# Kernel tuning notes

Hardware: AMD Instinct MI355X
Metric: run time of the kernel (lower is better)

## Reference

```python
import jax, jax.numpy as jnp
import numpy as np
from jax import lax

GRID_SIZE = 5
SPLINE_ORDER = 3
GRID_RANGE = (-1.0, 1.0)
# (cin, cout, kernel, stride, pad) per KAN conv layer
CONVS = [(3, 16, 7, 2, 3), (16, 32, 3, 2, 1), (32, 64, 3, 2, 1)]


def make_grid(in_features):
    # uniform extended knot grid: (in_features, grid_size + 2*order + 1)
    h = (GRID_RANGE[1] - GRID_RANGE[0]) / GRID_SIZE
    g = jnp.arange(-SPLINE_ORDER, GRID_SIZE + SPLINE_ORDER + 1, dtype=jnp.float32) * h + GRID_RANGE[0]
    return jnp.broadcast_to(g, (in_features, g.shape[0]))


def b_splines(x, grid):
    # x: (N, in)  ->  (N, in, grid_size + order) via Cox-de Boor recursion
    x = x[..., None]
    bases = ((x >= grid[:, :-1]) & (x < grid[:, 1:])).astype(x.dtype)
    for k in range(1, SPLINE_ORDER + 1):
        left = (x - grid[:, : -(k + 1)]) / (grid[:, k:-1] - grid[:, : -(k + 1)])
        right = (grid[:, k + 1:] - x) / (grid[:, k + 1:] - grid[:, 1:-k])
        bases = left * bases[..., :-1] + right * bases[..., 1:]
    return bases


def kan_linear(x, grid, base_w, spline_w, spline_scaler):
    # base path: silu(x) @ W_base^T ; spline path: B(x) contracted with scaled spline coeffs
    base = jax.nn.silu(x) @ base_w.T
    bsp = b_splines(x, grid)                      # (N, in, K)
    scaled = spline_w * spline_scaler[..., None]  # (out, in, K)
    spline = jnp.einsum('nik,oik->no', bsp, scaled)
    return base + spline


def max_pool_2x2(x):
    return lax.reduce_window(x, -jnp.inf, lax.max, (1, 1, 2, 2), (1, 1, 2, 2), 'VALID')


def setup_inputs() -> dict:
    key = jax.random.key(0)
    ks = jax.random.split(key, 16)
    inp = {'x': jax.random.uniform(ks[0], (8, 3, 224, 224), dtype=jnp.float32)}
    dims = [(16, 147), (32, 144), (64, 288)]
    i = 1
    for li, (out_f, in_f) in enumerate(dims):
        inp[f'bw{li}'] = jax.random.normal(ks[i], (out_f, in_f), jnp.float32) / np.sqrt(in_f); i += 1
        inp[f'sw{li}'] = jax.random.normal(ks[i], (out_f, in_f, GRID_SIZE + SPLINE_ORDER), jnp.float32) * 0.1; i += 1
        inp[f'sc{li}'] = 1.0 + 0.1 * jax.random.normal(ks[i], (out_f, in_f), jnp.float32); i += 1
    inp['bwc'] = jax.random.normal(ks[i], (200, 64), jnp.float32) / 8.0; i += 1
    inp['swc'] = jax.random.normal(ks[i], (200, 64, GRID_SIZE + SPLINE_ORDER), jnp.float32) * 0.1; i += 1
    inp['scc'] = 1.0 + 0.1 * jax.random.normal(ks[i], (200, 64), jnp.float32)
    return inp


def reference(x, bw0, sw0, sc0, bw1, sw1, sc1, bw2, sw2, sc2, bwc, swc, scc):
    params = [(bw0, sw0, sc0), (bw1, sw1, sc1), (bw2, sw2, sc2)]
    h = x
    for i, (cin, cout, k, s, p) in enumerate(CONVS):
        # unfold: (B, cin*k*k, Ho, Wo) with channel-major patch ordering (matches torch unfold)
        patches = lax.conv_general_dilated_patches(
            h, (k, k), (s, s), [(p, p), (p, p)],
            dimension_numbers=('NCHW', 'OIHW', 'NCHW'))
        B, F_, Ho, Wo = patches.shape
        flat = patches.transpose(0, 2, 3, 1).reshape(-1, F_)  # (B*Ho*Wo, cin*k*k)
        y = kan_linear(flat, make_grid(F_), *params[i])
        h = y.reshape(B, Ho, Wo, cout).transpose(0, 3, 1, 2)
        h = jax.nn.relu(h)
        if i < len(CONVS) - 1:
            h = max_pool_2x2(h)
    h = h.mean(axis=(2, 3))  # adaptive avg pool to 1x1 + flatten -> (B, 64)
    return kan_linear(h, make_grid(h.shape[1]), bwc, swc, scc)
```

## Files before the change

kernel.cpp:

```cpp
#include <hip/hip_runtime.h>

#define DEV __device__ __forceinline__

typedef _Float16 f16x8 __attribute__((ext_vector_type(8)));
typedef float f32x4 __attribute__((ext_vector_type(4)));
typedef unsigned int u32x4 __attribute__((ext_vector_type(4)));

DEV f16x8 kan_feats8(float x) {
    const float sil = x / (1.0f + __expf(-x));
    const float k0 = (float)(-3) * 0.4f - 1.0f;
    const float t = (x - k0) * 2.5f;
    const float mf = floorf(t);
    const int m = (int)mf;
    const float u = t - mf, v = 1.0f - u;
    const float u2 = u * u, u3 = u2 * u;
    const float N0 = v * v * v * (1.0f / 6.0f);
    const float N1 = (3.0f * u3 - 6.0f * u2 + 4.0f) * (1.0f / 6.0f);
    const float N2 = (-3.0f * u3 + 3.0f * u2 + 3.0f * u + 1.0f) * (1.0f / 6.0f);
    const float N3 = u3 * (1.0f / 6.0f);
    f16x8 g;
    g[0] = (_Float16)sil;
#pragma unroll
    for (int jj = 0; jj < 6; ++jj) {
        const int j = jj + 2;
        float val = 0.0f;
        val = (m == j + 3) ? N0 : val;
        val = (m == j + 2) ? N1 : val;
        val = (m == j + 1) ? N2 : val;
        val = (m == j)     ? N3 : val;
        g[1 + jj] = (_Float16)val;
    }
    g[7] = (_Float16)0.0f;
    return g;
}

DEV void kan_feats9(float x, float* f) {
    f[0] = x / (1.0f + __expf(-x));
    const float k0 = (float)(-3) * 0.4f - 1.0f;
    const float t = (x - k0) * 2.5f;
    const float mf = floorf(t);
    const int m = (int)mf;
    const float u = t - mf, v = 1.0f - u;
    const float u2 = u * u, u3 = u2 * u;
    const float N0 = v * v * v * (1.0f / 6.0f);
    const float N1 = (3.0f * u3 - 6.0f * u2 + 4.0f) * (1.0f / 6.0f);
    const float N2 = (-3.0f * u3 + 3.0f * u2 + 3.0f * u + 1.0f) * (1.0f / 6.0f);
    const float N3 = u3 * (1.0f / 6.0f);
#pragma unroll
    for (int j = 0; j < 8; ++j) {
        float val = 0.0f;
        val = (m == j + 3) ? N0 : val;
        val = (m == j + 2) ? N1 : val;
        val = (m == j + 1) ? N2 : val;
        val = (m == j)     ? N3 : val;
        f[1 + j] = val;
    }
}

__device__ constexpr int d_l0(int ii) {
    const int i = ii > 146 ? 146 : ii;
    const int ci = i / 49, rem = i % 49, kh = rem / 7, kw = rem % 7;
    return ((((kw & 1) * 3 + ci) * 13 + kh) * 19 + (kw >> 1)) * 16;
}
__device__ constexpr int d_l1(int i) {
    const int ch = i / 9, rem = i % 9, kh = rem / 3, kw = rem % 3;
    return ((((kw & 1) * 16 + ch) * 9 + kh) * 5 + (kw >> 1)) * 16;
}

template <int OUT_F, int IN_F>
DEV void pack_oct8(int g, const float* bw, const float* sw, const float* sc,
                   _Float16* W2) {
    const int o = g % OUT_F, i = g / OUT_F;
    f16x8 v;
    if (i < IN_F) {
        const int wi = o * IN_F + i;
        const float s = sc[wi];
        v[0] = (_Float16)bw[wi];
#pragma unroll
        for (int t = 1; t <= 6; ++t) v[t] = (_Float16)(sw[wi * 8 + t + 1] * s);
        v[7] = (_Float16)0.0f;
    } else {
#pragma unroll
        for (int t = 0; t < 8; ++t) v[t] = (_Float16)0.0f;
    }
    *(f16x8*)(W2 + g * 8) = v;
}

#define PS0 2368
#define PS1 4608
#define PS2 18432
#define PS3 12800
#define PS4 25088
#define PSUM (PS0 + PS1 + PS2 + PS3 + PS4)

__global__ __launch_bounds__(256) void prep_k(
    const float* __restrict__ bw0, const float* __restrict__ sw0, const float* __restrict__ sc0,
    const float* __restrict__ bw1, const float* __restrict__ sw1, const float* __restrict__ sc1,
    const float* __restrict__ bw2, const float* __restrict__ sw2, const float* __restrict__ sc2,
    const float* __restrict__ bwc, const float* __restrict__ swc, const float* __restrict__ scc,
    _Float16* __restrict__ W2_0, _Float16* __restrict__ W2_1, _Float16* __restrict__ W2_2,
    float* __restrict__ wcT, float* __restrict__ h2) {
    const int e = blockIdx.x * 256 + threadIdx.x;
    if (e < PS0) {
        pack_oct8<16, 147>(e, bw0, sw0, sc0, W2_0);
    } else if (e < PS0 + PS1) {
        pack_oct8<32, 144>(e - PS0, bw1, sw1, sc1, W2_1);
    } else if (e < PS0 + PS1 + PS2) {
        pack_oct8<64, 288>(e - PS0 - PS1, bw2, sw2, sc2, W2_2);
    } else if (e < PS0 + PS1 + PS2 + PS3) {
        const int ee = e - PS0 - PS1 - PS2;
        const int o = ee / 64, i = ee - o * 64;
        const float s = scc[ee];
        wcT[(i * 9 + 0) * 200 + o] = bwc[ee];
#pragma unroll
        for (int t = 0; t < 8; ++t)
            wcT[(i * 9 + 1 + t) * 200 + o] = swc[ee * 8 + t] * s;
    } else if (e < PSUM) {
        h2[e - PS0 - PS1 - PS2 - PS3] = 0.0f;
    }
}

__global__ __launch_bounds__(256, 5) void conv0_k(
    const float* __restrict__ x, const _Float16* __restrict__ W2,
    float* __restrict__ p0) {
    __shared__ __align__(16) _Float16 feats[1482 * 8];
    __shared__ float pb[4 * 8 * 16];
    const int tid = threadIdx.x;
    const int vt = blockIdx.x;
    const int b = vt / 196;
    const int r0 = vt - b * 196;
    const int bh = r0 / 7, bw = r0 - (r0 / 7) * 7;
    const int ih0 = bh * 8 - 3, iw0 = bw * 32 - 3;
    for (int t = tid; t < 1482; t += 256) {
        const int iwh = t % 19;
        int r = t / 19;
        const int ihp = r % 13; r /= 13;
        const int ci = r % 3;
        const int par = r / 3;
        const int ih = ih0 + ihp, iw = iw0 + 2 * iwh + par;
        float xv = 0.0f;
        if (ih >= 0 && ih < 224 && iw >= 0 && iw < 224)
            xv = x[((b * 3 + ci) * 224 + ih) * 224 + iw];
        *(f16x8*)(feats + t * 8) = kan_feats8(xv);
    }
    __syncthreads();
    const int lane = tid & 63, mt = tid >> 6;
    const int l15 = lane & 15, q = lane >> 4;
    const bool q1 = q & 1, q2 = q & 2;
    const char* aBase = (const char*)feats + ((2 * mt) * 19 + l15) * 16;
    const f16x8* __restrict__ Wv = (const f16x8*)W2;
    f32x4 acc = {0.f, 0.f, 0.f, 0.f};
#pragma unroll
    for (int s = 0; s < 37; ++s) {
        const int o0 = d_l0(4 * s), o1 = d_l0(4 * s + 1);
        const int o2 = d_l0(4 * s + 2), o3 = d_l0(4 * s + 3);
        const int e01 = q1 ? o1 : o0;
        const int e23 = q1 ? o3 : o2;
        const int aoff = q2 ? e23 : e01;
        const f16x8 a = *(const f16x8*)(aBase + aoff);
        const f16x8 bf = Wv[(s * 4 + q) * 16 + l15];
        acc = __builtin_amdgcn_mfma_f32_16x16x32_f16(a, bf, acc, 0, 0, 0);
    }
    pb[(mt * 8 + 2 * q + 0) * 16 + l15] = fmaxf(fmaxf(acc[0], 0.f), fmaxf(acc[1], 0.f));
    pb[(mt * 8 + 2 * q + 1) * 16 + l15] = fmaxf(fmaxf(acc[2], 0.f), fmaxf(acc[3], 0.f));
    __syncthreads();
    const int pr = tid >> 7, o = (tid >> 3) & 15, wp = tid & 7;
    const float v = fmaxf(pb[((2 * pr) * 8 + wp) * 16 + o],
                          pb[((2 * pr + 1) * 8 + wp) * 16 + o]);
    p0[((b * 16 + o) * 56 + bh * 2 + pr) * 56 + bw * 8 + wp] = v;
}

__global__ __launch_bounds__(256, 5) void conv1_k(
    const float* __restrict__ p0, const _Float16* __restrict__ W2,
    unsigned int* __restrict__ featP1) {
    __shared__ __align__(16) _Float16 feats[1440 * 8];
    __shared__ float abuf[2 * 32 * 16];
    const int tid = threadIdx.x;
    const int vt = blockIdx.x;
    const int b = vt / 49;
    const int r0 = vt - b * 49;
    const int bh = r0 / 7, bw = r0 - (r0 / 7) * 7;
    const int ih0 = bh * 8 - 1, iw0 = bw * 8 - 1;
    for (int t = tid; t < 1296; t += 256) {
        const int iwp = t % 9;
        int r = t / 9;
        const int ihp = r % 9;
        const int ch = r / 9;
        const int ih = ih0 + ihp, iw = iw0 + iwp;
        float xv = 0.0f;
        if (ih >= 0 && ih < 56 && iw >= 0 && iw < 56)
            xv = p0[((b * 16 + ch) * 56 + ih) * 56 + iw];
        const int slot = (((iwp & 1) * 16 + ch) * 9 + ihp) * 5 + (iwp >> 1);
        *(f16x8*)(feats + slot * 8) = kan_feats8(xv);
    }
    __syncthreads();
    const int lane = tid & 63, w = tid >> 6;
    const int kc = w >> 1, ot = w & 1;
    const int l15 = lane & 15, q = lane >> 4;
    const bool q1 = q & 1, q2 = q & 2;
    const int mh = l15 >> 2, mw = l15 & 3;
    const int ocol = ot * 16 + l15;
    const char* aBase = (const char*)feats + ((2 * mh) * 5 + mw) * 16 + kc * 5760;
    const f16x8* __restrict__ Wv = (const f16x8*)W2;
    f32x4 acc = {0.f, 0.f, 0.f, 0.f};
#pragma unroll
    for (int s = 0; s < 18; ++s) {
        const int o0 = d_l1(4 * s), o1 = d_l1(4 * s + 1);
        const int o2 = d_l1(4 * s + 2), o3 = d_l1(4 * s + 3);
        const int e01 = q1 ? o1 : o0;
        const int e23 = q1 ? o3 : o2;
        const int aoff = q2 ? e23 : e01;
        const f16x8 a = *(const f16x8*)(aBase + aoff);
        const f16x8 bf = Wv[(kc * 72 + s * 4 + q) * 32 + ocol];
        acc = __builtin_amdgcn_mfma_f32_16x16x32_f16(a, bf, acc, 0, 0, 0);
    }
#pragma unroll
    for (int reg = 0; reg < 4; ++reg)
        abuf[(kc * 32 + ocol) * 16 + q * 4 + reg] = acc[reg];
    __syncthreads();
    if (tid < 128) {
        const int o = tid >> 2, pp = tid & 3;
        const int hp = pp >> 1, wp = pp & 1;
        float mx = -1e30f;
#pragma unroll
        for (int dh = 0; dh < 2; ++dh)
#pragma unroll
            for (int dw = 0; dw < 2; ++dw) {
                const int m = (2 * hp + dh) * 4 + 2 * wp + dw;
                const float s = abuf[(0 * 32 + o) * 16 + m] + abuf[(1 * 32 + o) * 16 + m];
                mx = fmaxf(mx, fmaxf(s, 0.0f));
            }
        const f16x8 g = kan_feats8(mx);
        const size_t idx = ((b * 32 + o) * 14 + bh * 2 + hp) * 14 + bw * 2 + wp;
        *(u32x4*)(featP1 + idx * 4) = __builtin_bit_cast(u32x4, g);
    }
}

__global__ __launch_bounds__(256, 4) void conv2_k(
    const unsigned int* __restrict__ fm, const _Float16* __restrict__ W2,
    float* __restrict__ h2) {
    __shared__ __align__(16) unsigned int featW[16 * 132];
    const int tid = threadIdx.x;
    const int c = blockIdx.x % 9, rt = blockIdx.x / 9;
    const int lane = tid & 63, ot = tid >> 6;
    const int q = lane >> 4, l15 = lane & 15;
    const int ocol = ot * 16 + l15;
    const u32x4 F0p = __builtin_bit_cast(u32x4, kan_feats8(0.0f));
    const int i_in = tid & 31, rbase = tid >> 5;
    int hi0[2], wi0[2], pixb[2];
    bool rv[2];
#pragma unroll
    for (int t = 0; t < 2; ++t) {
        const int n = rt * 16 + rbase + t * 8;
        const int wo_ = n % 7, ho_ = (n / 7) % 7, b_ = n / 49;
        rv[t] = (n < 392);
        hi0[t] = ho_ * 2 - 1;
        wi0[t] = wo_ * 2 - 1;
        pixb[t] = b_ * 32 * 14 * 14;
    }
    f32x4 acc = {0.f, 0.f, 0.f, 0.f};
    const f16x8* __restrict__ Wv = (const f16x8*)W2;
    {
        const int ii = c * 32 + i_in;
        const int ci = ii / 9, rem = ii - ci * 9;
        const int kh = rem / 3, kw = rem - kh * 3;
#pragma unroll
        for (int t = 0; t < 2; ++t) {
            const int hi = hi0[t] + kh, wi = wi0[t] + kw;
            const bool v = rv[t] && hi >= 0 && hi < 14 && wi >= 0 && wi < 14;
            u32x4 rec = F0p;
            if (v)
                rec = *(const u32x4*)(fm + (size_t)(pixb[t] + (ci * 14 + hi) * 14 + wi) * 4);
            *(u32x4*)(featW + (rbase + t * 8) * 132 + i_in * 4) = rec;
        }
        __syncthreads();
        const char* arow = (const char*)featW + l15 * 528 + q * 16;
#pragma unroll
        for (int s = 0; s < 8; ++s) {
            const f16x8 a = *(const f16x8*)(arow + s * 64);
            const f16x8 bf = Wv[(c * 32 + s * 4 + q) * 64 + ocol];
            acc = __builtin_amdgcn_mfma_f32_16x16x32_f16(a, bf, acc, 0, 0, 0);
        }
    }
#pragma unroll
    for (int reg = 0; reg < 4; ++reg) {
        const int n = rt * 16 + q * 4 + reg;
        if (n < 392) {
            const int wo_ = n % 7, ho_ = (n / 7) % 7, b_ = n / 49;
            atomicAdd(h2 + ((b_ * 64 + ocol) * 7 + ho_) * 7 + wo_, acc[reg]);
        }
    }
}

__global__ __launch_bounds__(256) void head_k(
    const float* __restrict__ h2, const float* __restrict__ wT,
    float* __restrict__ out) {
    __shared__ float feat[576];
    __shared__ float psum[4 * 64];
    const int tid = threadIdx.x;
    const int n = blockIdx.x >> 2, oc = blockIdx.x & 3;
    if (tid < 64) {
        const float* p = h2 + (n * 64 + tid) * 49;
        float s = 0.0f;
        for (int j = 0; j < 49; ++j) s += fmaxf(p[j], 0.0f);
        float f9[9];
        kan_feats9(s / 49.0f, f9);
#pragma unroll
        for (int t = 0; t < 9; ++t) feat[tid * 9 + t] = f9[t];
    }
    __syncthreads();
    const int js = tid >> 6, ol = tid & 63;
    if (ol < 50) {
        const int o = oc * 50 + ol;
        float sum = 0.0f;
        for (int j = js * 144; j < js * 144 + 144; ++j)
            sum += feat[j] * wT[j * 200 + o];
        psum[js * 64 + ol] = sum;
    }
    __syncthreads();
    if (tid < 50)
        out[n * 200 + oc * 50 + tid] =
            psum[tid] + psum[64 + tid] + psum[128 + tid] + psum[192 + tid];
}

extern "C" void kernel_launch(void* const* d_in, const int* in_sizes, int n_in,
                              void* d_out, int out_size, void* d_ws, size_t ws_size,
                              hipStream_t stream) {
    const float* x   = (const float*)d_in[0];
    const float* bw0 = (const float*)d_in[1];
    const float* sw0 = (const float*)d_in[2];
    const float* sc0 = (const float*)d_in[3];
    const float* bw1 = (const float*)d_in[4];
    const float* sw1 = (const float*)d_in[5];
    const float* sc1 = (const float*)d_in[6];
    const float* bw2 = (const float*)d_in[7];
    const float* sw2 = (const float*)d_in[8];
    const float* sc2 = (const float*)d_in[9];
    const float* bwc = (const float*)d_in[10];
    const float* swc = (const float*)d_in[11];
    const float* scc = (const float*)d_in[12];
    float* out = (float*)d_out;

    char* ws = (char*)d_ws;
    size_t off = 0;
    auto alloc = [&](size_t nbytes) {
        char* p = ws + off;
        off += (nbytes + 255) & ~(size_t)255;
        return p;
    };
    _Float16* W2_0 = (_Float16*)alloc(PS0 * 16);
    _Float16* W2_1 = (_Float16*)alloc(PS1 * 16);
    _Float16* W2_2 = (_Float16*)alloc(PS2 * 16);
    float* wcT = (float*)alloc(576 * 200 * 4);
    float* h2  = (float*)alloc(8 * 64 * 49 * 4);
    float* p0  = (float*)alloc((size_t)8 * 16 * 56 * 56 * 4);
    unsigned int* featP1 = (unsigned int*)alloc((size_t)8 * 32 * 14 * 14 * 16);

    prep_k<<<(PSUM + 255) / 256, 256, 0, stream>>>(
        bw0, sw0, sc0, bw1, sw1, sc1, bw2, sw2, sc2, bwc, swc, scc,
        W2_0, W2_1, W2_2, wcT, h2);
    conv0_k<<<1568, 256, 0, stream>>>(x, W2_0, p0);
    conv1_k<<<392, 256, 0, stream>>>(p0, W2_1, featP1);
    conv2_k<<<225, 256, 0, stream>>>(featP1, W2_2, h2);
    head_k<<<32, 256, 0, stream>>>(h2, wcT, out);
}
```

Baseline: 122.9 us.

## Halve conv0 grid with two tiles per block and emit precomputed KAN features

```diff
diff --git a/kernel.cpp b/kernel.cpp
--- a/kernel.cpp
+++ b/kernel.cpp
@@ -122,56 +122,75 @@
 
 __global__ __launch_bounds__(256, 5) void conv0_k(
     const float* __restrict__ x, const _Float16* __restrict__ W2,
-    float* __restrict__ p0) {
+    unsigned int* __restrict__ featP0) {
     __shared__ __align__(16) _Float16 feats[1482 * 8];
     __shared__ float pb[4 * 8 * 16];
     const int tid = threadIdx.x;
-    const int vt = blockIdx.x;
-    const int b = vt / 196;
-    const int r0 = vt - b * 196;
-    const int bh = r0 / 7, bw = r0 - (r0 / 7) * 7;
-    const int ih0 = bh * 8 - 3, iw0 = bw * 32 - 3;
-    for (int t = tid; t < 1482; t += 256) {
-        const int iwh = t % 19;
-        int r = t / 19;
-        const int ihp = r % 13; r /= 13;
-        const int ci = r % 3;
-        const int par = r / 3;
-        const int ih = ih0 + ihp, iw = iw0 + 2 * iwh + par;
-        float xv = 0.0f;
-        if (ih >= 0 && ih < 224 && iw >= 0 && iw < 224)
-            xv = x[((b * 3 + ci) * 224 + ih) * 224 + iw];
-        *(f16x8*)(feats + t * 8) = kan_feats8(xv);
-    }
-    __syncthreads();
+    const int bb = blockIdx.x;
+
+    auto featurize = [&](int vt) {
+        const int b = vt / 196;
+        const int r0 = vt - b * 196;
+        const int bh = r0 / 7, bw_ = r0 - (r0 / 7) * 7;
+        const int ih0 = bh * 8 - 3, iw0 = bw_ * 32 - 3;
+        for (int t = tid; t < 1482; t += 256) {
+            const int iwa = t % 38;
+            const int rr = t / 38;
+            const int ihp = rr % 13, ci = rr / 13;
+            const int ih = ih0 + ihp, iw = iw0 + iwa;
+            float xv = 0.0f;
+            if (ih >= 0 && ih < 224 && iw >= 0 && iw < 224)
+                xv = x[((b * 3 + ci) * 224 + ih) * 224 + iw];
+            const int slot = (((iwa & 1) * 3 + ci) * 13 + ihp) * 19 + (iwa >> 1);
+            *(f16x8*)(feats + slot * 8) = kan_feats8(xv);
+        }
+    };
+
+    featurize(bb);
+    __syncthreads();
+
     const int lane = tid & 63, mt = tid >> 6;
     const int l15 = lane & 15, q = lane >> 4;
     const bool q1 = q & 1, q2 = q & 2;
     const char* aBase = (const char*)feats + ((2 * mt) * 19 + l15) * 16;
     const f16x8* __restrict__ Wv = (const f16x8*)W2;
-    f32x4 acc = {0.f, 0.f, 0.f, 0.f};
-#pragma unroll
-    for (int s = 0; s < 37; ++s) {
-        const int o0 = d_l0(4 * s), o1 = d_l0(4 * s + 1);
-        const int o2 = d_l0(4 * s + 2), o3 = d_l0(4 * s + 3);
-        const int e01 = q1 ? o1 : o0;
-        const int e23 = q1 ? o3 : o2;
-        const int aoff = q2 ? e23 : e01;
-        const f16x8 a = *(const f16x8*)(aBase + aoff);
-        const f16x8 bf = Wv[(s * 4 + q) * 16 + l15];
-        acc = __builtin_amdgcn_mfma_f32_16x16x32_f16(a, bf, acc, 0, 0, 0);
-    }
-    pb[(mt * 8 + 2 * q + 0) * 16 + l15] = fmaxf(fmaxf(acc[0], 0.f), fmaxf(acc[1], 0.f));
-    pb[(mt * 8 + 2 * q + 1) * 16 + l15] = fmaxf(fmaxf(acc[2], 0.f), fmaxf(acc[3], 0.f));
-    __syncthreads();
-    const int pr = tid >> 7, o = (tid >> 3) & 15, wp = tid & 7;
-    const float v = fmaxf(pb[((2 * pr) * 8 + wp) * 16 + o],
-                          pb[((2 * pr + 1) * 8 + wp) * 16 + o]);
-    p0[((b * 16 + o) * 56 + bh * 2 + pr) * 56 + bw * 8 + wp] = v;
+
+#pragma unroll 1
+    for (int rep = 0; rep < 2; ++rep) {
+        const int vt = bb + rep * 784;
+        f32x4 acc = {0.f, 0.f, 0.f, 0.f};
+#pragma unroll
+        for (int s = 0; s < 37; ++s) {
+            const int o0 = d_l0(4 * s), o1 = d_l0(4 * s + 1);
+            const int o2 = d_l0(4 * s + 2), o3 = d_l0(4 * s + 3);
+            const int e01 = q1 ? o1 : o0;
+            const int e23 = q1 ? o3 : o2;
+            const int aoff = q2 ? e23 : e01;
+            const f16x8 a = *(const f16x8*)(aBase + aoff);
+            const f16x8 bf = Wv[(s * 4 + q) * 16 + l15];
+            acc = __builtin_amdgcn_mfma_f32_16x16x32_f16(a, bf, acc, 0, 0, 0);
+        }
+        pb[(mt * 8 + 2 * q + 0) * 16 + l15] = fmaxf(fmaxf(acc[0], 0.f), fmaxf(acc[1], 0.f));
+        pb[(mt * 8 + 2 * q + 1) * 16 + l15] = fmaxf(fmaxf(acc[2], 0.f), fmaxf(acc[3], 0.f));
+        __syncthreads();
+        if (rep == 0) featurize(bb + 784);
+        {
+            const int b = vt / 196;
+            const int r0 = vt - b * 196;
+            const int bh = r0 / 7, bw_ = r0 - (r0 / 7) * 7;
+            const int pr = tid >> 7, o = (tid >> 3) & 15, wp = tid & 7;
+            const float v = fmaxf(pb[((2 * pr) * 8 + wp) * 16 + o],
+                                  pb[((2 * pr + 1) * 8 + wp) * 16 + o]);
+            const f16x8 g = kan_feats8(v);
+            const size_t idx = ((size_t)(b * 16 + o) * 56 + bh * 2 + pr) * 56 + bw_ * 8 + wp;
+            *(u32x4*)(featP0 + idx * 4) = __builtin_bit_cast(u32x4, g);
+        }
+        __syncthreads();
+    }
 }
 
 __global__ __launch_bounds__(256, 5) void conv1_k(
-    const float* __restrict__ p0, const _Float16* __restrict__ W2,
+    const unsigned int* __restrict__ featP0, const _Float16* __restrict__ W2,
     unsigned int* __restrict__ featP1) {
     __shared__ __align__(16) _Float16 feats[1440 * 8];
     __shared__ float abuf[2 * 32 * 16];
@@ -181,17 +200,19 @@
     const int r0 = vt - b * 49;
     const int bh = r0 / 7, bw = r0 - (r0 / 7) * 7;
     const int ih0 = bh * 8 - 1, iw0 = bw * 8 - 1;
+    const u32x4 F0p = __builtin_bit_cast(u32x4, kan_feats8(0.0f));
     for (int t = tid; t < 1296; t += 256) {
         const int iwp = t % 9;
         int r = t / 9;
         const int ihp = r % 9;
         const int ch = r / 9;
         const int ih = ih0 + ihp, iw = iw0 + iwp;
-        float xv = 0.0f;
+        u32x4 rec = F0p;
         if (ih >= 0 && ih < 56 && iw >= 0 && iw < 56)
-            xv = p0[((b * 16 + ch) * 56 + ih) * 56 + iw];
+            rec = *(const u32x4*)(featP0 +
+                    (size_t)(((b * 16 + ch) * 56 + ih) * 56 + iw) * 4);
         const int slot = (((iwp & 1) * 16 + ch) * 9 + ihp) * 5 + (iwp >> 1);
-        *(f16x8*)(feats + slot * 8) = kan_feats8(xv);
+        *(u32x4*)((unsigned int*)feats + slot * 4) = rec;
     }
     __syncthreads();
     const int lane = tid & 63, w = tid >> 6;
@@ -353,14 +374,14 @@
     _Float16* W2_2 = (_Float16*)alloc(PS2 * 16);
     float* wcT = (float*)alloc(576 * 200 * 4);
     float* h2  = (float*)alloc(8 * 64 * 49 * 4);
-    float* p0  = (float*)alloc((size_t)8 * 16 * 56 * 56 * 4);
+    unsigned int* featP0 = (unsigned int*)alloc((size_t)8 * 16 * 56 * 56 * 16);
     unsigned int* featP1 = (unsigned int*)alloc((size_t)8 * 32 * 14 * 14 * 16);
 
     prep_k<<<(PSUM + 255) / 256, 256, 0, stream>>>(
         bw0, sw0, sc0, bw1, sw1, sc1, bw2, sw2, sc2, bwc, swc, scc,
         W2_0, W2_1, W2_2, wcT, h2);
-    conv0_k<<<1568, 256, 0, stream>>>(x, W2_0, p0);
-    conv1_k<<<392, 256, 0, stream>>>(p0, W2_1, featP1);
+    conv0_k<<<784, 256, 0, stream>>>(x, W2_0, featP0);
+    conv1_k<<<392, 256, 0, stream>>>(featP0, W2_1, featP1);
     conv2_k<<<225, 256, 0, stream>>>(featP1, W2_2, h2);
     head_k<<<32, 256, 0, stream>>>(h2, wcT, out);
 }
```

Measured after the change: 165.6 us. 34.7% more time.
